# Kernel tuning notes

Measured on AMD Instinct MI355X. Metric: run time of the kernel, lower is better.

## Reference

```python
import jax, jax.numpy as jnp
import numpy as np

N_NODES = 100000
N_FEAT = 128
HIDDEN = 128
N_EDGES = 1600000


def _glorot(key, shape):
    fan_in, fan_out = shape[1], shape[0]
    lim = float(np.sqrt(6.0 / (fan_in + fan_out)))
    return jax.random.uniform(key, shape, jnp.float32, -lim, lim)


def setup_inputs() -> dict:
    key = jax.random.key(0)
    ks = jax.random.split(key, 9)
    x = jax.random.normal(ks[0], (N_NODES, N_FEAT), jnp.float32)
    edge_index = jax.random.randint(ks[1], (2, N_EDGES), 0, N_NODES, jnp.int64)
    return {
        "x": x,
        "edge_index": edge_index,
        # GraphConv layer 1: lin_rel (with bias) + lin_root (no bias)
        "W1_rel": _glorot(ks[2], (HIDDEN, N_FEAT)),
        "b1": jnp.zeros((HIDDEN,), jnp.float32),
        "W1_root": _glorot(ks[3], (HIDDEN, N_FEAT)),
        # layer 2
        "W2_rel": _glorot(ks[4], (HIDDEN, HIDDEN)),
        "b2": jnp.zeros((HIDDEN,), jnp.float32),
        "W2_root": _glorot(ks[5], (HIDDEN, HIDDEN)),
        # layer 3 -> scalar
        "W3_rel": _glorot(ks[6], (1, HIDDEN)),
        "b3": jnp.zeros((1,), jnp.float32),
        "W3_root": _glorot(ks[7], (1, HIDDEN)),
    }


def _graph_conv(x, src, dst, W_rel, b_rel, W_root):
    # PyG GraphConv, aggr='add': out_i = W_rel @ (sum_{j->i} x_j) + b_rel + W_root @ x_i
    agg = jax.ops.segment_sum(x[src], dst, num_segments=x.shape[0])  # [N, F_in]
    return agg @ W_rel.T + b_rel + x @ W_root.T


def reference(x, edge_index, W1_rel, b1, W1_root, W2_rel, b2, W2_root, W3_rel, b3, W3_root):
    src, dst = edge_index[0], edge_index[1]
    h = jax.nn.relu(_graph_conv(x, src, dst, W1_rel, b1, W1_root))
    h = jax.nn.relu(_graph_conv(h, src, dst, W2_rel, b2, W2_root))
    h = _graph_conv(h, src, dst, W3_rel, b3, W3_root)  # [N, 1]
    # global_mean_pool with batch = zeros -> mean over all nodes -> [1, 1]
    return jnp.mean(h, axis=0, keepdims=True)
```

## Files before the change

### kernel.cpp

```cpp
#include <hip/hip_runtime.h>

#define NN 100000
#define NF 128
#define NE 1600000
#define NBK 782
#define CH 4096
#define BINB 391
#define MAXB 2816
#define RED_B 512
#define NGB 1563
#define CVTXB 12500

typedef unsigned short ushort_t;
typedef unsigned char uchar_t;
typedef __attribute__((ext_vector_type(8))) short bf16x8;
typedef __attribute__((ext_vector_type(4))) float f32x4;
typedef __attribute__((ext_vector_type(2))) float f32x2;

__device__ inline ushort_t f2bf(float f) {
  union { float f; unsigned u; } v; v.f = f;
  const unsigned r = v.u + 0x7FFFu + ((v.u >> 16) & 1u);
  return (ushort_t)(r >> 16);
}
__device__ inline float bf2f(ushort_t h) {
  union { unsigned u; float f; } v; v.u = ((unsigned)h) << 16;
  return v.f;
}

__device__ inline void block_scan(const int* hist, int* lofs, int* wsum) {
  const int t = threadIdx.x;
  const int b4 = t * 4;
  const int h0 = hist[b4], h1 = hist[b4 + 1], h2 = hist[b4 + 2], h3 = hist[b4 + 3];
  const int tsum = h0 + h1 + h2 + h3;
  const int lane = t & 63, w = t >> 6;
  int s = tsum;
#pragma unroll
  for (int o = 1; o < 64; o <<= 1) {
    const int u = __shfl_up(s, o);
    if (lane >= o) s += u;
  }
  if (lane == 63) wsum[w] = s;
  __syncthreads();
  int add = 0;
  for (int i = 0; i < w; ++i) add += wsum[i];
  const int ex = add + s - tsum;
  lofs[b4] = ex;
  lofs[b4 + 1] = ex + h0;
  lofs[b4 + 2] = ex + h0 + h1;
  lofs[b4 + 3] = ex + h0 + h1 + h2;
}

__global__ __launch_bounds__(256) void k_prep(
    const int* __restrict__ src, const int* __restrict__ dst,
    int* __restrict__ bcursor, int* __restrict__ packed,
    const float* __restrict__ x, ushort_t* __restrict__ xb,
    unsigned* __restrict__ x8,
    const float* __restrict__ w0, const float* __restrict__ w1,
    const float* __restrict__ w2, const float* __restrict__ w3,
    ushort_t* __restrict__ wout) {
  __shared__ int hist[1024];
  __shared__ int lofs[1024];
  __shared__ int wsum[4];
  __shared__ int gofs[NBK];
  __shared__ int list[CH];
  __shared__ unsigned short blist[CH];
  const int blk = blockIdx.x;
  const int t = threadIdx.x;

  if (blk >= BINB + 64) {
    const int i = (blk - BINB - 64) * 256 + t;
    const float4 v = *reinterpret_cast<const float4*>(x + (size_t)i * 4);
    ushort4 o;
    o.x = f2bf(v.x); o.y = f2bf(v.y); o.z = f2bf(v.z); o.w = f2bf(v.w);
    *reinterpret_cast<ushort4*>(xb + (size_t)i * 4) = o;
    int u8 = __builtin_amdgcn_cvt_pk_fp8_f32(v.x, v.y, 0, false);
    u8 = __builtin_amdgcn_cvt_pk_fp8_f32(v.z, v.w, u8, true);
    x8[i] = (unsigned)u8;
    return;
  }
  if (blk >= BINB) {
    const int i = (blk - BINB) * 256 + t;
    wout[i] = f2bf(w0[i]);
    wout[16384 + i] = f2bf(w1[i]);
    wout[32768 + i] = f2bf(w2[i]);
    wout[49152 + i] = f2bf(w3[i]);
    return;
  }

  const int e0 = blk * CH;
  const int n = min(CH, NE - e0);

  for (int i = t; i < 1024; i += 256) hist[i] = 0;
  __syncthreads();
  for (int i = t; i < n; i += 256) atomicAdd(&hist[dst[e0 + i] >> 7], 1);
  __syncthreads();
  block_scan(hist, lofs, wsum);
  __syncthreads();
  for (int b = t; b < NBK; b += 256) {
    const int cnt = hist[b];
    gofs[b] = cnt ? atomicAdd(&bcursor[b], cnt) : 0;
    hist[b] = 0;
  }
  __syncthreads();
  for (int i = t; i < n; i += 256) {
    const int d = dst[e0 + i];
    const int s = src[e0 + i];
    const int b = d >> 7;
    const int r = atomicAdd(&hist[b], 1);
    const int q = lofs[b] + r;
    list[q] = ((d & 127) << 17) | s;
    blist[q] = (unsigned short)b;
  }
  __syncthreads();
  for (int q = t; q < n; q += 256) {
    const int b = blist[q];
    const int idx = gofs[b] + (q - lofs[b]);
    if (idx < MAXB) packed[b * MAXB + idx] = list[q];
  }
}

__global__ __launch_bounds__(256) void k_sort2(int* __restrict__ packed,
                                               const int* __restrict__ bcursor,
                                               int* __restrict__ offs,
                                               int* __restrict__ ends) {
  __shared__ int plist[MAXB];
  __shared__ int slist[MAXB];
  __shared__ int hist[128];
  __shared__ int lofs[128];
  __shared__ int wsum2[2];
  const int b = blockIdx.x, t = threadIdx.x;
  const int beg = b * MAXB;
  const int n = min(bcursor[b], MAXB);

  for (int i = t; i < n; i += 256) plist[i] = packed[beg + i];
  if (t < 128) hist[t] = 0;
  __syncthreads();
  for (int i = t; i < n; i += 256) atomicAdd(&hist[plist[i] >> 17], 1);
  __syncthreads();
  int s = (t < 128) ? hist[t] : 0;
  {
    const int lane = t & 63;
#pragma unroll
    for (int o = 1; o < 64; o <<= 1) {
      const int u = __shfl_up(s, o);
      if (lane >= o) s += u;
    }
    if (t < 128 && lane == 63) wsum2[t >> 6] = s;
  }
  __syncthreads();
  if (t < 128) {
    const int ex = s - hist[t] + ((t >= 64) ? wsum2[0] : 0);
    lofs[t] = ex;
    const int node = (b << 7) + t;
    if (node < NN) {
      offs[node] = beg + ex;
      ends[node] = beg + ex + hist[t];
    }
    hist[t] = 0;
  }
  __syncthreads();
  for (int i = t; i < n; i += 256) {
    const int p = plist[i];
    const int ld = p >> 17;
    const int r = atomicAdd(&hist[ld], 1);
    slist[lofs[ld] + r] = p & 0x1FFFF;
  }
  __syncthreads();
  for (int i = t; i < n; i += 256) packed[beg + i] = slist[i];
}

__global__ __launch_bounds__(256) void k_agg8(const uchar_t* __restrict__ f8,
                                              const int* __restrict__ offs,
                                              const int* __restrict__ ends,
                                              const int* __restrict__ srcs,
                                              ushort_t* __restrict__ out) {
  const int lane = threadIdx.x & 63;
  const int wid = threadIdx.x >> 6;
  const int node = blockIdx.x * 8 + wid * 2 + (lane >> 5);
  if (node >= NN) return;
  const int c = (lane & 31) * 4;
  const int beg = offs[node];
  const int end = ends[node];

  float x0 = 0.f, y0 = 0.f, z0 = 0.f, w0 = 0.f;
  float x1 = 0.f, y1 = 0.f, z1 = 0.f, w1 = 0.f;
  float x2 = 0.f, y2 = 0.f, z2 = 0.f, w2 = 0.f;
  float x3 = 0.f, y3 = 0.f, z3 = 0.f, w3 = 0.f;
  float x4 = 0.f, y4 = 0.f, z4 = 0.f, w4 = 0.f;
  float x5 = 0.f, y5 = 0.f, z5 = 0.f, w5 = 0.f;
  float x6 = 0.f, y6 = 0.f, z6 = 0.f, w6 = 0.f;
  float x7 = 0.f, y7 = 0.f, z7 = 0.f, w7 = 0.f;

  int e = beg;
  for (; e + 8 <= end; e += 8) {
    const int s0 = srcs[e], s1 = srcs[e + 1], s2 = srcs[e + 2], s3 = srcs[e + 3];
    const int s4 = srcs[e + 4], s5 = srcs[e + 5], s6 = srcs[e + 6], s7 = srcs[e + 7];
    const unsigned u0 = *(const unsigned*)(f8 + s0 * NF + c);
    const unsigned u1 = *(const unsigned*)(f8 + s1 * NF + c);
    const unsigned u2 = *(const unsigned*)(f8 + s2 * NF + c);
    const unsigned u3 = *(const unsigned*)(f8 + s3 * NF + c);
    const unsigned u4 = *(const unsigned*)(f8 + s4 * NF + c);
    const unsigned u5 = *(const unsigned*)(f8 + s5 * NF + c);
    const unsigned u6 = *(const unsigned*)(f8 + s6 * NF + c);
    const unsigned u7 = *(const unsigned*)(f8 + s7 * NF + c);
    {
      const f32x2 a = __builtin_amdgcn_cvt_pk_f32_fp8((int)u0, false);
      const f32x2 b = __builtin_amdgcn_cvt_pk_f32_fp8((int)u0, true);
      x0 += a[0]; y0 += a[1]; z0 += b[0]; w0 += b[1];
    }
    {
      const f32x2 a = __builtin_amdgcn_cvt_pk_f32_fp8((int)u1, false);
      const f32x2 b = __builtin_amdgcn_cvt_pk_f32_fp8((int)u1, true);
      x1 += a[0]; y1 += a[1]; z1 += b[0]; w1 += b[1];
    }
    {
      const f32x2 a = __builtin_amdgcn_cvt_pk_f32_fp8((int)u2, false);
      const f32x2 b = __builtin_amdgcn_cvt_pk_f32_fp8((int)u2, true);
      x2 += a[0]; y2 += a[1]; z2 += b[0]; w2 += b[1];
    }
    {
      const f32x2 a = __builtin_amdgcn_cvt_pk_f32_fp8((int)u3, false);
      const f32x2 b = __builtin_amdgcn_cvt_pk_f32_fp8((int)u3, true);
      x3 += a[0]; y3 += a[1]; z3 += b[0]; w3 += b[1];
    }
    {
      const f32x2 a = __builtin_amdgcn_cvt_pk_f32_fp8((int)u4, false);
      const f32x2 b = __builtin_amdgcn_cvt_pk_f32_fp8((int)u4, true);
      x4 += a[0]; y4 += a[1]; z4 += b[0]; w4 += b[1];
    }
    {
      const f32x2 a = __builtin_amdgcn_cvt_pk_f32_fp8((int)u5, false);
      const f32x2 b = __builtin_amdgcn_cvt_pk_f32_fp8((int)u5, true);
      x5 += a[0]; y5 += a[1]; z5 += b[0]; w5 += b[1];
    }
    {
      const f32x2 a = __builtin_amdgcn_cvt_pk_f32_fp8((int)u6, false);
      const f32x2 b = __builtin_amdgcn_cvt_pk_f32_fp8((int)u6, true);
      x6 += a[0]; y6 += a[1]; z6 += b[0]; w6 += b[1];
    }
    {
      const f32x2 a = __builtin_amdgcn_cvt_pk_f32_fp8((int)u7, false);
      const f32x2 b = __builtin_amdgcn_cvt_pk_f32_fp8((int)u7, true);
      x7 += a[0]; y7 += a[1]; z7 += b[0]; w7 += b[1];
    }
  }
  for (; e + 2 <= end; e += 2) {
    const int s0 = srcs[e], s1 = srcs[e + 1];
    const unsigned u0 = *(const unsigned*)(f8 + s0 * NF + c);
    const unsigned u1 = *(const unsigned*)(f8 + s1 * NF + c);
    {
      const f32x2 a = __builtin_amdgcn_cvt_pk_f32_fp8((int)u0, false);
      const f32x2 b = __builtin_amdgcn_cvt_pk_f32_fp8((int)u0, true);
      x0 += a[0]; y0 += a[1]; z0 += b[0]; w0 += b[1];
    }
    {
      const f32x2 a = __builtin_amdgcn_cvt_pk_f32_fp8((int)u1, false);
      const f32x2 b = __builtin_amdgcn_cvt_pk_f32_fp8((int)u1, true);
      x1 += a[0]; y1 += a[1]; z1 += b[0]; w1 += b[1];
    }
  }
  for (; e < end; ++e) {
    const unsigned u = *(const unsigned*)(f8 + srcs[e] * NF + c);
    const f32x2 a = __builtin_amdgcn_cvt_pk_f32_fp8((int)u, false);
    const f32x2 b = __builtin_amdgcn_cvt_pk_f32_fp8((int)u, true);
    x0 += a[0]; y0 += a[1]; z0 += b[0]; w0 += b[1];
  }
  ushort4 r;
  r.x = f2bf(((x0 + x1) + (x2 + x3)) + ((x4 + x5) + (x6 + x7)));
  r.y = f2bf(((y0 + y1) + (y2 + y3)) + ((y4 + y5) + (y6 + y7)));
  r.z = f2bf(((z0 + z1) + (z2 + z3)) + ((z4 + z5) + (z6 + z7)));
  r.w = f2bf(((w0 + w1) + (w2 + w3)) + ((w4 + w5) + (w6 + w7)));
  *(ushort4*)(out + node * NF + c) = r;
}

template <int MODE>
__global__ __launch_bounds__(256) void k_gemm(const ushort_t* __restrict__ A1,
                                              const ushort_t* __restrict__ A2,
                                              const ushort_t* __restrict__ B1,
                                              const ushort_t* __restrict__ B2,
                                              const float* __restrict__ bias,
                                              ushort_t* __restrict__ out,
                                              uchar_t* __restrict__ out8,
                                              const float* __restrict__ W3rel,
                                              const float* __restrict__ W3root,
                                              float* __restrict__ y1,
                                              float* __restrict__ P2) {
  __shared__ ushort_t As[64][264];
  __shared__ float y1s[4][64];
  __shared__ float y2s[4][64];
  const int tid = threadIdx.x;
  const int lane = tid & 63;
  const int wid = tid >> 6;
  const int bm = blockIdx.x * 64;

  const int jb = wid * 32 + (lane & 15);
  const int kc = (lane >> 4) * 8;
  bf16x8 bfrag[2][8];
#pragma unroll
  for (int nt = 0; nt < 2; ++nt) {
    const int j = jb + nt * 16;
#pragma unroll
    for (int ks = 0; ks < 4; ++ks) {
      bfrag[nt][ks] = *reinterpret_cast<const bf16x8*>(B1 + j * 128 + ks * 32 + kc);
      bfrag[nt][ks + 4] = *reinterpret_cast<const bf16x8*>(B2 + j * 128 + ks * 32 + kc);
    }
  }

  {
    const int r = tid >> 2, p = tid & 3;
    const int node = bm + r;
#pragma unroll
    for (int s = 0; s < 2; ++s) {
      const ushort_t* __restrict__ sp = s ? A2 : A1;
#pragma unroll
      for (int q = 0; q < 4; ++q) {
        const int col = p * 32 + q * 8;
        bf16x8 v = (node < NN) ? *reinterpret_cast<const bf16x8*>(sp + node * 128 + col)
                               : (bf16x8)(short)0;
        *reinterpret_cast<bf16x8*>(&As[r][s * 128 + col]) = v;
      }
    }
  }
  __syncthreads();

  f32x4 acc[4][2];
#pragma unroll
  for (int mt = 0; mt < 4; ++mt) {
    acc[mt][0] = (f32x4)0.f;
    acc[mt][1] = (f32x4)0.f;
  }

  const int ar = lane & 15;
#pragma unroll
  for (int ks = 0; ks < 8; ++ks) {
#pragma unroll
    for (int mt = 0; mt < 4; ++mt) {
      const bf16x8 a = *reinterpret_cast<const bf16x8*>(&As[mt * 16 + ar][ks * 32 + kc]);
      acc[mt][0] = __builtin_amdgcn_mfma_f32_16x16x32_bf16(a, bfrag[0][ks], acc[mt][0], 0, 0, 0);
      acc[mt][1] = __builtin_amdgcn_mfma_f32_16x16x32_bf16(a, bfrag[1][ks], acc[mt][1], 0, 0, 0);
    }
  }

  const int rg = (lane >> 4) * 4;
  if (MODE == 0) {
#pragma unroll
    for (int nt = 0; nt < 2; ++nt) {
      const int j = jb + nt * 16;
      const float bv = bias[j];
#pragma unroll
      for (int mt = 0; mt < 4; ++mt) {
#pragma unroll
        for (int r = 0; r < 4; ++r) {
          const int node = bm + mt * 16 + rg + r;
          if (node < NN) {
            const float v = fmaxf(acc[mt][nt][r] + bv, 0.f);
            out[node * 128 + j] = f2bf(v);
            const int u8 = __builtin_amdgcn_cvt_pk_fp8_f32(v, v, 0, false);
            out8[node * 128 + j] = (uchar_t)(u8 & 0xFF);
          }
        }
      }
    }
  } else {
    const float bv0 = bias[jb], bv1 = bias[jb + 16];
    const float wr0 = W3rel[jb], wr1 = W3rel[jb + 16];
    const float wt0 = W3root[jb], wt1 = W3root[jb + 16];
#pragma unroll
    for (int mt = 0; mt < 4; ++mt) {
#pragma unroll
      for (int r = 0; r < 4; ++r) {
        const float v0 = fmaxf(acc[mt][0][r] + bv0, 0.f);
        const float v1 = fmaxf(acc[mt][1][r] + bv1, 0.f);
        float s1 = v0 * wr0 + v1 * wr1;
        float s2 = v0 * wt0 + v1 * wt1;
#pragma unroll
        for (int o = 1; o < 16; o <<= 1) {
          s1 += __shfl_xor(s1, o);
          s2 += __shfl_xor(s2, o);
        }
        if ((lane & 15) == 0) {
          const int nloc = mt * 16 + rg + r;
          y1s[wid][nloc] = s1;
          y2s[wid][nloc] = s2;
        }
      }
    }
    __syncthreads();
    if (tid < 64) {
      const int node = bm + tid;
      const float s1 = (y1s[0][tid] + y1s[1][tid]) + (y1s[2][tid] + y1s[3][tid]);
      float p = (node < NN)
                    ? (y2s[0][tid] + y2s[1][tid]) + (y2s[2][tid] + y2s[3][tid])
                    : 0.f;
      if (node < NN) y1[node] = s1;
#pragma unroll
      for (int o = 32; o > 0; o >>= 1) p += __shfl_down(p, o);
      if (tid == 0) P2[blockIdx.x] = p;
    }
  }
}

__global__ __launch_bounds__(256) void k_esum(const int* __restrict__ src,
                                              const float* __restrict__ y1,
                                              float* __restrict__ P1) {
  float p = 0.f;
  const int stride = RED_B * 256;
  for (int e = blockIdx.x * 256 + threadIdx.x; e < NE; e += stride)
    p += y1[src[e]];
#pragma unroll
  for (int o = 32; o > 0; o >>= 1) p += __shfl_down(p, o);
  __shared__ float tmp[4];
  const int lane = threadIdx.x & 63, w = threadIdx.x >> 6;
  if (lane == 0) tmp[w] = p;
  __syncthreads();
  if (threadIdx.x == 0)
    P1[blockIdx.x] = (tmp[0] + tmp[1]) + (tmp[2] + tmp[3]);
}

__global__ __launch_bounds__(256) void k_final(const float* __restrict__ P1,
                                               const float* __restrict__ P2,
                                               const float* __restrict__ b3,
                                               float* __restrict__ out) {
  const int t = threadIdx.x;
  float v = P1[t] + P1[t + 256];
  for (int i = t; i < NGB; i += 256) v += P2[i];
#pragma unroll
  for (int o = 32; o > 0; o >>= 1) v += __shfl_down(v, o);
  __shared__ float tmp[4];
  if ((t & 63) == 0) tmp[t >> 6] = v;
  __syncthreads();
  if (t == 0)
    out[0] = ((tmp[0] + tmp[1]) + (tmp[2] + tmp[3])) * (1.0f / NN) + b3[0];
}

extern "C" void kernel_launch(void* const* d_in, const int* in_sizes, int n_in,
                              void* d_out, int out_size, void* d_ws, size_t ws_size,
                              hipStream_t stream) {
  const float* x = (const float*)d_in[0];
  const int* ei = (const int*)d_in[1];
  const float* W1rel = (const float*)d_in[2];
  const float* b1 = (const float*)d_in[3];
  const float* W1root = (const float*)d_in[4];
  const float* W2rel = (const float*)d_in[5];
  const float* b2 = (const float*)d_in[6];
  const float* W2root = (const float*)d_in[7];
  const float* W3rel = (const float*)d_in[8];
  const float* b3 = (const float*)d_in[9];
  const float* W3root = (const float*)d_in[10];

  const int* src = ei;
  const int* dst = ei + NE;

  char* ws = (char*)d_ws;
  size_t off = 0;
  ushort_t* xb   = (ushort_t*)(ws + off); off += (size_t)NN * NF * 2;
  ushort_t* h1b  = (ushort_t*)(ws + off); off += (size_t)NN * NF * 2;
  ushort_t* aggb = (ushort_t*)(ws + off); off += (size_t)NN * NF * 2;
  uchar_t* x8    = (uchar_t*)(ws + off);  off += (size_t)NN * NF;
  ushort_t* Wb   = (ushort_t*)(ws + off); off += 65536 * 2;
  int* offs    = (int*)(ws + off); off += (size_t)NN * 4;
  int* ends    = (int*)(ws + off); off += (size_t)NN * 4;
  float* y1    = (float*)(ws + off); off += (size_t)NN * 4;
  int* bcursor = (int*)(ws + off); off += 1024 * 4;
  float* P1    = (float*)(ws + off); off += RED_B * 4;
  float* P2    = (float*)(ws + off); off += 2048 * 4;
  int* packed  = (int*)(ws + off); off += (size_t)NBK * MAXB * 4;
  int* srcs    = packed;
  uchar_t* h1f8 = x8;
  float* outp = (float*)d_out;

  hipMemsetAsync(bcursor, 0, 1024 * sizeof(int), stream);

  k_prep<<<BINB + 64 + CVTXB, 256, 0, stream>>>(src, dst, bcursor, packed,
                                                x, xb, (unsigned*)x8,
                                                W1rel, W1root, W2rel, W2root, Wb);
  k_sort2<<<NBK, 256, 0, stream>>>(packed, bcursor, offs, ends);

  k_agg8<<<(NN + 7) / 8, 256, 0, stream>>>(x8, offs, ends, srcs, aggb);
  k_gemm<0><<<NGB, 256, 0, stream>>>(aggb, xb, Wb, Wb + 16384, b1, h1b, h1f8,
                                     nullptr, nullptr, nullptr, nullptr);

  k_agg8<<<(NN + 7) / 8, 256, 0, stream>>>(h1f8, offs, ends, srcs, aggb);
  k_gemm<1><<<NGB, 256, 0, stream>>>(aggb, h1b, Wb + 32768, Wb + 49152, b2,
                                     nullptr, nullptr, W3rel, W3root, y1, P2);

  k_esum<<<RED_B, 256, 0, stream>>>(src, y1, P1);
  k_final<<<1, 256, 0, stream>>>(P1, P2, b3, outp);
}
```

Before: 201.3 us.

## Store aggregation and GEMM operands in fp8 instead of bf16

```diff
diff --git a/kernel.cpp b/kernel.cpp
--- a/kernel.cpp
+++ b/kernel.cpp
@@ -9,7 +9,7 @@
 #define MAXB 2816
 #define RED_B 512
 #define NGB 1563
-#define CVTXB 12500
+#define CVTX8B 6250
 
 typedef unsigned short ushort_t;
 typedef unsigned char uchar_t;
@@ -22,9 +22,13 @@
   const unsigned r = v.u + 0x7FFFu + ((v.u >> 16) & 1u);
   return (ushort_t)(r >> 16);
 }
-__device__ inline float bf2f(ushort_t h) {
-  union { unsigned u; float f; } v; v.u = ((unsigned)h) << 16;
-  return v.f;
+
+__device__ inline ushort4 f8x4_bf(unsigned u) {
+  const f32x2 a = __builtin_amdgcn_cvt_pk_f32_fp8((int)u, false);
+  const f32x2 b = __builtin_amdgcn_cvt_pk_f32_fp8((int)u, true);
+  ushort4 r;
+  r.x = f2bf(a[0]); r.y = f2bf(a[1]); r.z = f2bf(b[0]); r.w = f2bf(b[1]);
+  return r;
 }
 
 __device__ inline void block_scan(const int* hist, int* lofs, int* wsum) {
@@ -53,8 +57,7 @@
 __global__ __launch_bounds__(256) void k_prep(
     const int* __restrict__ src, const int* __restrict__ dst,
     int* __restrict__ bcursor, int* __restrict__ packed,
-    const float* __restrict__ x, ushort_t* __restrict__ xb,
-    unsigned* __restrict__ x8,
+    const float* __restrict__ x, unsigned* __restrict__ x8u,
     const float* __restrict__ w0, const float* __restrict__ w1,
     const float* __restrict__ w2, const float* __restrict__ w3,
     ushort_t* __restrict__ wout) {
@@ -68,14 +71,15 @@
   const int t = threadIdx.x;
 
   if (blk >= BINB + 64) {
-    const int i = (blk - BINB - 64) * 256 + t;
-    const float4 v = *reinterpret_cast<const float4*>(x + (size_t)i * 4);
-    ushort4 o;
-    o.x = f2bf(v.x); o.y = f2bf(v.y); o.z = f2bf(v.z); o.w = f2bf(v.w);
-    *reinterpret_cast<ushort4*>(xb + (size_t)i * 4) = o;
-    int u8 = __builtin_amdgcn_cvt_pk_fp8_f32(v.x, v.y, 0, false);
-    u8 = __builtin_amdgcn_cvt_pk_fp8_f32(v.z, v.w, u8, true);
-    x8[i] = (unsigned)u8;
+    const size_t i = (size_t)(blk - BINB - 64) * 256 + t;
+    const float4 v0 = *reinterpret_cast<const float4*>(x + i * 8);
+    const float4 v1 = *reinterpret_cast<const float4*>(x + i * 8 + 4);
+    int lo = __builtin_amdgcn_cvt_pk_fp8_f32(v0.x, v0.y, 0, false);
+    lo = __builtin_amdgcn_cvt_pk_fp8_f32(v0.z, v0.w, lo, true);
+    int hi = __builtin_amdgcn_cvt_pk_fp8_f32(v1.x, v1.y, 0, false);
+    hi = __builtin_amdgcn_cvt_pk_fp8_f32(v1.z, v1.w, hi, true);
+    uint2 o; o.x = (unsigned)lo; o.y = (unsigned)hi;
+    *reinterpret_cast<uint2*>(x8u + i * 2) = o;
     return;
   }
   if (blk >= BINB) {
@@ -173,7 +177,7 @@
                                               const int* __restrict__ offs,
                                               const int* __restrict__ ends,
                                               const int* __restrict__ srcs,
-                                              ushort_t* __restrict__ out) {
+                                              uchar_t* __restrict__ out8) {
   const int lane = threadIdx.x & 63;
   const int wid = threadIdx.x >> 6;
   const int node = blockIdx.x * 8 + wid * 2 + (lane >> 5);
@@ -265,21 +269,21 @@
     const f32x2 b = __builtin_amdgcn_cvt_pk_f32_fp8((int)u, true);
     x0 += a[0]; y0 += a[1]; z0 += b[0]; w0 += b[1];
   }
-  ushort4 r;
-  r.x = f2bf(((x0 + x1) + (x2 + x3)) + ((x4 + x5) + (x6 + x7)));
-  r.y = f2bf(((y0 + y1) + (y2 + y3)) + ((y4 + y5) + (y6 + y7)));
-  r.z = f2bf(((z0 + z1) + (z2 + z3)) + ((z4 + z5) + (z6 + z7)));
-  r.w = f2bf(((w0 + w1) + (w2 + w3)) + ((w4 + w5) + (w6 + w7)));
-  *(ushort4*)(out + node * NF + c) = r;
+  const float X = ((x0 + x1) + (x2 + x3)) + ((x4 + x5) + (x6 + x7));
+  const float Y = ((y0 + y1) + (y2 + y3)) + ((y4 + y5) + (y6 + y7));
+  const float Z = ((z0 + z1) + (z2 + z3)) + ((z4 + z5) + (z6 + z7));
+  const float W = ((w0 + w1) + (w2 + w3)) + ((w4 + w5) + (w6 + w7));
+  int o = __builtin_amdgcn_cvt_pk_fp8_f32(X, Y, 0, false);
+  o = __builtin_amdgcn_cvt_pk_fp8_f32(Z, W, o, true);
+  *(unsigned*)(out8 + node * NF + c) = (unsigned)o;
 }
 
 template <int MODE>
-__global__ __launch_bounds__(256) void k_gemm(const ushort_t* __restrict__ A1,
-                                              const ushort_t* __restrict__ A2,
+__global__ __launch_bounds__(256) void k_gemm(const uchar_t* __restrict__ A1,
+                                              const uchar_t* __restrict__ A2,
                                               const ushort_t* __restrict__ B1,
                                               const ushort_t* __restrict__ B2,
                                               const float* __restrict__ bias,
-                                              ushort_t* __restrict__ out,
                                               uchar_t* __restrict__ out8,
                                               const float* __restrict__ W3rel,
                                               const float* __restrict__ W3root,
@@ -311,14 +315,21 @@
     const int node = bm + r;
 #pragma unroll
     for (int s = 0; s < 2; ++s) {
-      const ushort_t* __restrict__ sp = s ? A2 : A1;
-#pragma unroll
-      for (int q = 0; q < 4; ++q) {
-        const int col = p * 32 + q * 8;
-        bf16x8 v = (node < NN) ? *reinterpret_cast<const bf16x8*>(sp + node * 128 + col)
-                               : (bf16x8)(short)0;
-        *reinterpret_cast<bf16x8*>(&As[r][s * 128 + col]) = v;
+      const uchar_t* __restrict__ sp = s ? A2 : A1;
+      uint4 q0 = make_uint4(0u, 0u, 0u, 0u), q1 = q0;
+      if (node < NN) {
+        q0 = *reinterpret_cast<const uint4*>(sp + (size_t)node * 128 + p * 32);
+        q1 = *reinterpret_cast<const uint4*>(sp + (size_t)node * 128 + p * 32 + 16);
       }
+      const int col = s * 128 + p * 32;
+      *reinterpret_cast<ushort4*>(&As[r][col + 0]) = f8x4_bf(q0.x);
+      *reinterpret_cast<ushort4*>(&As[r][col + 4]) = f8x4_bf(q0.y);
+      *reinterpret_cast<ushort4*>(&As[r][col + 8]) = f8x4_bf(q0.z);
+      *reinterpret_cast<ushort4*>(&As[r][col + 12]) = f8x4_bf(q0.w);
+      *reinterpret_cast<ushort4*>(&As[r][col + 16]) = f8x4_bf(q1.x);
+      *reinterpret_cast<ushort4*>(&As[r][col + 20]) = f8x4_bf(q1.y);
+      *reinterpret_cast<ushort4*>(&As[r][col + 24]) = f8x4_bf(q1.z);
+      *reinterpret_cast<ushort4*>(&As[r][col + 28]) = f8x4_bf(q1.w);
     }
   }
   __syncthreads();
@@ -354,9 +365,8 @@
           const int node = bm + mt * 16 + rg + r;
           if (node < NN) {
             const float v = fmaxf(acc[mt][nt][r] + bv, 0.f);
-            out[node * 128 + j] = f2bf(v);
             const int u8 = __builtin_amdgcn_cvt_pk_fp8_f32(v, v, 0, false);
-            out8[node * 128 + j] = (uchar_t)(u8 & 0xFF);
+            out8[(size_t)node * 128 + j] = (uchar_t)(u8 & 0xFF);
           }
         }
       }
@@ -453,10 +463,8 @@
 
   char* ws = (char*)d_ws;
   size_t off = 0;
-  ushort_t* xb   = (ushort_t*)(ws + off); off += (size_t)NN * NF * 2;
-  ushort_t* h1b  = (ushort_t*)(ws + off); off += (size_t)NN * NF * 2;
-  ushort_t* aggb = (ushort_t*)(ws + off); off += (size_t)NN * NF * 2;
   uchar_t* x8    = (uchar_t*)(ws + off);  off += (size_t)NN * NF;
+  uchar_t* agg8  = (uchar_t*)(ws + off);  off += (size_t)NN * NF;
   ushort_t* Wb   = (ushort_t*)(ws + off); off += 65536 * 2;
   int* offs    = (int*)(ws + off); off += (size_t)NN * 4;
   int* ends    = (int*)(ws + off); off += (size_t)NN * 4;
@@ -471,18 +479,18 @@
 
   hipMemsetAsync(bcursor, 0, 1024 * sizeof(int), stream);
 
-  k_prep<<<BINB + 64 + CVTXB, 256, 0, stream>>>(src, dst, bcursor, packed,
-                                                x, xb, (unsigned*)x8,
-                                                W1rel, W1root, W2rel, W2root, Wb);
+  k_prep<<<BINB + 64 + CVTX8B, 256, 0, stream>>>(src, dst, bcursor, packed,
+                                                 x, (unsigned*)x8,
+                                                 W1rel, W1root, W2rel, W2root, Wb);
   k_sort2<<<NBK, 256, 0, stream>>>(packed, bcursor, offs, ends);
 
-  k_agg8<<<(NN + 7) / 8, 256, 0, stream>>>(x8, offs, ends, srcs, aggb);
-  k_gemm<0><<<NGB, 256, 0, stream>>>(aggb, xb, Wb, Wb + 16384, b1, h1b, h1f8,
+  k_agg8<<<(NN + 7) / 8, 256, 0, stream>>>(x8, offs, ends, srcs, agg8);
+  k_gemm<0><<<NGB, 256, 0, stream>>>(agg8, x8, Wb, Wb + 16384, b1, h1f8,
                                      nullptr, nullptr, nullptr, nullptr);
 
-  k_agg8<<<(NN + 7) / 8, 256, 0, stream>>>(h1f8, offs, ends, srcs, aggb);
-  k_gemm<1><<<NGB, 256, 0, stream>>>(aggb, h1b, Wb + 32768, Wb + 49152, b2,
-                                     nullptr, nullptr, W3rel, W3root, y1, P2);
+  k_agg8<<<(NN + 7) / 8, 256, 0, stream>>>(h1f8, offs, ends, srcs, agg8);
+  k_gemm<1><<<NGB, 256, 0, stream>>>(agg8, h1f8, Wb + 32768, Wb + 49152, b2,
+                                     nullptr, W3rel, W3root, y1, P2);
 
   k_esum<<<RED_B, 256, 0, stream>>>(src, y1, P1);
   k_final<<<1, 256, 0, stream>>>(P1, P2, b3, outp);
```

Result: faster. 190.5 us, median of 2 (-5.3%).
